# Performance work log

Hardware: AMD Instinct MI355X
Metric: run time of the kernel (lower is better)

Reference implementation:

```python
import jax, jax.numpy as jnp
import numpy as np

N_NODES = 100000


def _lightgcn_layer(x, src, dst, norm):
    # message: norm * x[src]; aggregate: mean over incoming edges at dst
    msg = norm[:, None] * x[src]                                   # [E+N, D]
    s = jax.ops.segment_sum(msg, dst, num_segments=N_NODES)        # [N, D]
    cnt = jax.ops.segment_sum(jnp.ones_like(norm), dst, num_segments=N_NODES)
    return s / cnt[:, None]                                        # deg>=1 due to self-loops


def _graph_embeddings(emb, edge_index):
    n = emb.shape[0]
    loop = jnp.arange(n, dtype=edge_index.dtype)
    src = jnp.concatenate([edge_index[0], loop])                   # self-loops appended
    dst = jnp.concatenate([edge_index[1], loop])
    deg = jax.ops.segment_sum(jnp.ones(src.shape[0], emb.dtype), src, num_segments=N_NODES)
    dis = deg ** -0.5
    norm = dis[src] * dis[dst]
    x = emb
    acc = emb
    for _ in range(2):  # num_layers
        x = _lightgcn_layer(x, src, dst, norm)
        acc = acc + x
    return acc / 3.0  # mean over (num_layers + 1) embeddings


def setup_inputs() -> dict:
    key = jax.random.key(0)
    k1, k2, k3, k4 = jax.random.split(key, 4)
    emb = jax.random.normal(k1, (N_NODES, 128), dtype=jnp.float32) * 0.02
    edge_index = jax.random.randint(k2, (2, 600000), 0, N_NODES, dtype=jnp.int64)
    items = jax.random.randint(k3, (4096, 1), 0, N_NODES, dtype=jnp.int64)
    samples = jax.random.randint(k4, (4096, 100), 0, N_NODES, dtype=jnp.int64)
    return {"emb": emb, "edge_index": edge_index, "items": items, "samples": samples}


def reference(emb, edge_index, items, samples):
    embeddings = _graph_embeddings(emb, edge_index)                # [N, D]
    item_emb = embeddings[items]                                   # [B, 1, D]
    sample_emb = embeddings[samples]                               # [B, S, D]
    scores = jnp.einsum('bod,bsd->bos', item_emb, sample_emb)      # [B, 1, S]
    return scores.squeeze(1)                                       # [B, S]
```

## Files before the change

### kernel.cpp

```cpp
#include <hip/hip_runtime.h>

#define NN 100000
#define D 128
#define W 32
#define NX 8

__device__ __forceinline__ unsigned short f2bf(float f) {
    unsigned u = __float_as_uint(f);
    u += 0x7FFF + ((u >> 16) & 1);
    return (unsigned short)(u >> 16);
}
__device__ __forceinline__ float bf2f(unsigned short h) {
    return __uint_as_float(((unsigned)h) << 16);
}
__device__ __forceinline__ unsigned pack2(float a, float b) {
    return (unsigned)f2bf(a) | ((unsigned)f2bf(b) << 16);
}

__global__ __launch_bounds__(256) void fillcount_kernel(const int* __restrict__ src,
                                                        const int* __restrict__ dst,
                                                        int* __restrict__ degR,
                                                        int* __restrict__ fillc,
                                                        int* __restrict__ ell, int E) {
    int xcc = __builtin_amdgcn_s_getreg(20 | (3 << 11)) & (NX - 1);
    int e = blockIdx.x * 256 + threadIdx.x;
    if (e < E) {
        int s = src[e], d = dst[e];
        __hip_atomic_fetch_add(&degR[(size_t)xcc * NN + s], 1,
                               __ATOMIC_RELAXED, __HIP_MEMORY_SCOPE_WORKGROUP);
        int pos = atomicAdd(&fillc[d], 1);
        if (pos < W) ell[(size_t)d * W + pos] = s;
    }
}

__global__ __launch_bounds__(256) void invert_kernel(const int* __restrict__ degR,
                                                     float* __restrict__ dis,
                                                     float* __restrict__ disinv, int n) {
    int i = blockIdx.x * 256 + threadIdx.x;
    if (i < n) {
        int dsum = 0;
        #pragma unroll
        for (int r = 0; r < NX; ++r) dsum += degR[(size_t)r * NN + i];
        float dp1 = (float)(dsum + 1);
        dis[i] = rsqrtf(dp1);
        disinv[i] = sqrtf(dp1);
    }
}

__global__ __launch_bounds__(256) void convert_kernel(const float* __restrict__ in,
                                                      const float* __restrict__ dis,
                                                      unsigned short* __restrict__ outh,
                                                      int total8) {
    int t = blockIdx.x * 256 + threadIdx.x;
    if (t >= total8) return;
    float sc = dis[t >> 4];
    const float4 a = ((const float4*)in)[t * 2];
    const float4 b = ((const float4*)in)[t * 2 + 1];
    uint4 o;
    o.x = pack2(sc * a.x, sc * a.y);
    o.y = pack2(sc * a.z, sc * a.w);
    o.z = pack2(sc * b.x, sc * b.y);
    o.w = pack2(sc * b.z, sc * b.w);
    ((uint4*)outh)[t] = o;
}

template <bool FUSE>
__global__ __launch_bounds__(256) void gather_kernel(const int* __restrict__ ell,
                                                     const int* __restrict__ fillc,
                                                     const unsigned short* __restrict__ yh,
                                                     const float* __restrict__ emb,
                                                     const float* __restrict__ dis,
                                                     const float* __restrict__ disinv,
                                                     unsigned short* __restrict__ outh, int n) {
    unsigned t = blockIdx.x * 256u + threadIdx.x;
    unsigned i = t >> 5, q = t & 31u;
    if (i >= (unsigned)n) return;
    int len = fillc[i];
    int lenc = len > W ? W : len;
    const int* base = ell + (size_t)i * W;
    const ushort4 ph = *(const ushort4*)(yh + (size_t)i * D + q * 4);
    float sx = bf2f(ph.x), sy = bf2f(ph.y), sz = bf2f(ph.z), sw = bf2f(ph.w);
    float4 acc = {sx, sy, sz, sw};
    int j = 0;
    for (; j + 4 <= lenc; j += 4) {
        const int4 ss = *(const int4*)(base + j);
        const ushort4 v0 = *(const ushort4*)(yh + (size_t)ss.x * D + q * 4);
        const ushort4 v1 = *(const ushort4*)(yh + (size_t)ss.y * D + q * 4);
        const ushort4 v2 = *(const ushort4*)(yh + (size_t)ss.z * D + q * 4);
        const ushort4 v3 = *(const ushort4*)(yh + (size_t)ss.w * D + q * 4);
        acc.x += (bf2f(v0.x) + bf2f(v1.x)) + (bf2f(v2.x) + bf2f(v3.x));
        acc.y += (bf2f(v0.y) + bf2f(v1.y)) + (bf2f(v2.y) + bf2f(v3.y));
        acc.z += (bf2f(v0.z) + bf2f(v1.z)) + (bf2f(v2.z) + bf2f(v3.z));
        acc.w += (bf2f(v0.w) + bf2f(v1.w)) + (bf2f(v2.w) + bf2f(v3.w));
    }
    for (; j < lenc; ++j) {
        int s0 = base[j];
        const ushort4 v0 = *(const ushort4*)(yh + (size_t)s0 * D + q * 4);
        acc.x += bf2f(v0.x);
        acc.y += bf2f(v0.y);
        acc.z += bf2f(v0.z);
        acc.w += bf2f(v0.w);
    }
    float ds = dis[i];
    float ci = 1.0f / (float)(len + 1);
    ushort4 o;
    if (!FUSE) {
        float f1 = ci * ds * ds;
        o.x = f2bf(f1 * acc.x);
        o.y = f2bf(f1 * acc.y);
        o.z = f2bf(f1 * acc.z);
        o.w = f2bf(f1 * acc.w);
    } else {
        float g = ci * ds;
        float dvi = disinv[i];
        const float4 e = *(const float4*)(emb + (size_t)i * D + q * 4);
        const float k = 1.0f / 3.0f;
        o.x = f2bf((e.x + sx * dvi + g * acc.x) * k);
        o.y = f2bf((e.y + sy * dvi + g * acc.y) * k);
        o.z = f2bf((e.z + sz * dvi + g * acc.z) * k);
        o.w = f2bf((e.w + sw * dvi + g * acc.w) * k);
    }
    *(ushort4*)(outh + (size_t)i * D + q * 4) = o;
}

__global__ __launch_bounds__(256) void scores_kernel(const unsigned short* __restrict__ finh,
                                                     const int* __restrict__ items,
                                                     const int* __restrict__ samples,
                                                     float* __restrict__ out, int S) {
    __shared__ float it[D];
    int b = blockIdx.x;
    if (threadIdx.x < D) it[threadIdx.x] = bf2f(finh[(size_t)items[b] * D + threadIdx.x]);
    __syncthreads();
    int hw = threadIdx.x >> 5, lane = threadIdx.x & 31;
    const float4 w = *(const float4*)(it + lane * 4);
    int s = hw;
    for (; s + 8 < S; s += 16) {
        int node0 = samples[b * S + s];
        int node1 = samples[b * S + s + 8];
        const ushort4 v0 = *(const ushort4*)(finh + (size_t)node0 * D + lane * 4);
        const ushort4 v1 = *(const ushort4*)(finh + (size_t)node1 * D + lane * 4);
        float a0 = bf2f(v0.x) * w.x + bf2f(v0.y) * w.y + bf2f(v0.z) * w.z + bf2f(v0.w) * w.w;
        float a1 = bf2f(v1.x) * w.x + bf2f(v1.y) * w.y + bf2f(v1.z) * w.z + bf2f(v1.w) * w.w;
        #pragma unroll
        for (int o = 16; o; o >>= 1) {
            a0 += __shfl_xor(a0, o);
            a1 += __shfl_xor(a1, o);
        }
        if (lane == 0) {
            out[b * S + s] = a0;
            out[b * S + s + 8] = a1;
        }
    }
    if (s < S) {
        int node = samples[b * S + s];
        const ushort4 v = *(const ushort4*)(finh + (size_t)node * D + lane * 4);
        float acc = bf2f(v.x) * w.x + bf2f(v.y) * w.y + bf2f(v.z) * w.z + bf2f(v.w) * w.w;
        #pragma unroll
        for (int o = 16; o; o >>= 1) acc += __shfl_xor(acc, o);
        if (lane == 0) out[b * S + s] = acc;
    }
}

extern "C" void kernel_launch(void* const* d_in, const int* in_sizes, int n_in,
                              void* d_out, int out_size, void* d_ws, size_t ws_size,
                              hipStream_t stream) {
    const float* emb = (const float*)d_in[0];
    const int* ei = (const int*)d_in[1];
    const int* items = (const int*)d_in[2];
    const int* samples = (const int*)d_in[3];
    float* out = (float*)d_out;

    const int E = in_sizes[1] / 2;
    const int B = in_sizes[2];
    const int S = in_sizes[3] / B;
    const int* src = ei;
    const int* dst = ei + E;

    int* degR = (int*)d_ws;
    int* fillc = degR + (size_t)NX * NN;
    float* dis = (float*)(fillc + NN);
    float* disinv = dis + NN;
    int* ell = (int*)(disinv + NN);
    size_t off = (size_t)(ell + (size_t)NN * W - (int*)d_ws);
    off = (off + 3) & ~(size_t)3;
    unsigned short* embh = (unsigned short*)((int*)d_ws + off);
    unsigned short* x1h = embh + (size_t)NN * D;
    unsigned short* finh = x1h + (size_t)NN * D;

    hipMemsetAsync(degR, 0, (NX + 1) * NN * sizeof(int), stream);

    fillcount_kernel<<<(E + 255) / 256, 256, 0, stream>>>(src, dst, degR, fillc, ell, E);
    invert_kernel<<<(NN + 255) / 256, 256, 0, stream>>>(degR, dis, disinv, NN);

    convert_kernel<<<((NN * D / 8) + 255) / 256, 256, 0, stream>>>(emb, dis, embh, NN * D / 8);

    const int gblocks = (NN * 32 + 255) / 256;
    gather_kernel<false><<<gblocks, 256, 0, stream>>>(ell, fillc, embh, emb, dis, disinv, x1h, NN);
    gather_kernel<true><<<gblocks, 256, 0, stream>>>(ell, fillc, x1h, emb, dis, disinv, finh, NN);

    scores_kernel<<<B, 256, 0, stream>>>(finh, items, samples, out, S);
}
```

Before: 174.1 us.

## Merge edge counting with bf16 conversion and compute degree weights inside gather

The edge fill/degree-count pass and the fp32-to-bf16 embedding conversion now run as one heterogeneous launch, split by block index. Because the conversion no longer needs the degree normalization, the separate invert kernel and the per-XCC degree replicas are removed. The first gather applies rsqrt(deg+1) for each neighbor on the fly, which adds a scattered deg load and an rsqrt per edge. Degree atomics are now plain global atomics on a single array, which may increase contention compared with the XCC-replicated counters.

```diff
diff --git a/kernel.cpp b/kernel.cpp
--- a/kernel.cpp
+++ b/kernel.cpp
@@ -3,7 +3,6 @@
 #define NN 100000
 #define D 128
 #define W 32
-#define NX 8
 
 __device__ __forceinline__ unsigned short f2bf(float f) {
     unsigned u = __float_as_uint(f);
@@ -17,77 +16,109 @@
     return (unsigned)f2bf(a) | ((unsigned)f2bf(b) << 16);
 }
 
-__global__ __launch_bounds__(256) void fillcount_kernel(const int* __restrict__ src,
-                                                        const int* __restrict__ dst,
-                                                        int* __restrict__ degR,
-                                                        int* __restrict__ fillc,
-                                                        int* __restrict__ ell, int E) {
-    int xcc = __builtin_amdgcn_s_getreg(20 | (3 << 11)) & (NX - 1);
-    int e = blockIdx.x * 256 + threadIdx.x;
-    if (e < E) {
-        int s = src[e], d = dst[e];
-        __hip_atomic_fetch_add(&degR[(size_t)xcc * NN + s], 1,
-                               __ATOMIC_RELAXED, __HIP_MEMORY_SCOPE_WORKGROUP);
-        int pos = atomicAdd(&fillc[d], 1);
-        if (pos < W) ell[(size_t)d * W + pos] = s;
-    }
-}
-
-__global__ __launch_bounds__(256) void invert_kernel(const int* __restrict__ degR,
-                                                     float* __restrict__ dis,
-                                                     float* __restrict__ disinv, int n) {
-    int i = blockIdx.x * 256 + threadIdx.x;
-    if (i < n) {
-        int dsum = 0;
-        #pragma unroll
-        for (int r = 0; r < NX; ++r) dsum += degR[(size_t)r * NN + i];
-        float dp1 = (float)(dsum + 1);
-        dis[i] = rsqrtf(dp1);
-        disinv[i] = sqrtf(dp1);
-    }
-}
-
-__global__ __launch_bounds__(256) void convert_kernel(const float* __restrict__ in,
-                                                      const float* __restrict__ dis,
-                                                      unsigned short* __restrict__ outh,
-                                                      int total8) {
-    int t = blockIdx.x * 256 + threadIdx.x;
-    if (t >= total8) return;
-    float sc = dis[t >> 4];
-    const float4 a = ((const float4*)in)[t * 2];
-    const float4 b = ((const float4*)in)[t * 2 + 1];
-    uint4 o;
-    o.x = pack2(sc * a.x, sc * a.y);
-    o.y = pack2(sc * a.z, sc * a.w);
-    o.z = pack2(sc * b.x, sc * b.y);
-    o.w = pack2(sc * b.z, sc * b.w);
-    ((uint4*)outh)[t] = o;
-}
-
-template <bool FUSE>
-__global__ __launch_bounds__(256) void gather_kernel(const int* __restrict__ ell,
-                                                     const int* __restrict__ fillc,
-                                                     const unsigned short* __restrict__ yh,
+__global__ __launch_bounds__(256) void hetero_kernel(const int* __restrict__ src,
+                                                     const int* __restrict__ dst,
                                                      const float* __restrict__ emb,
-                                                     const float* __restrict__ dis,
-                                                     const float* __restrict__ disinv,
-                                                     unsigned short* __restrict__ outh, int n) {
+                                                     int* __restrict__ deg,
+                                                     int* __restrict__ fillc,
+                                                     int* __restrict__ ell,
+                                                     unsigned short* __restrict__ y0h,
+                                                     int E, int EB, int total8) {
+    int b = blockIdx.x;
+    if (b < EB) {
+        int e = b * 256 + threadIdx.x;
+        if (e < E) {
+            int s = src[e], d = dst[e];
+            atomicAdd(&deg[s], 1);
+            int pos = atomicAdd(&fillc[d], 1);
+            if (pos < W) ell[(size_t)d * W + pos] = s;
+        }
+    } else {
+        int t = (b - EB) * 256 + threadIdx.x;
+        if (t < total8) {
+            const float4 a = ((const float4*)emb)[t * 2];
+            const float4 c = ((const float4*)emb)[t * 2 + 1];
+            uint4 o;
+            o.x = pack2(a.x, a.y);
+            o.y = pack2(a.z, a.w);
+            o.z = pack2(c.x, c.y);
+            o.w = pack2(c.z, c.w);
+            ((uint4*)y0h)[t] = o;
+        }
+    }
+}
+
+__global__ __launch_bounds__(256) void gather1_kernel(const int* __restrict__ ell,
+                                                      const int* __restrict__ fillc,
+                                                      const int* __restrict__ deg,
+                                                      const unsigned short* __restrict__ y0h,
+                                                      unsigned short* __restrict__ y1h, int n) {
     unsigned t = blockIdx.x * 256u + threadIdx.x;
     unsigned i = t >> 5, q = t & 31u;
     if (i >= (unsigned)n) return;
     int len = fillc[i];
     int lenc = len > W ? W : len;
     const int* base = ell + (size_t)i * W;
-    const ushort4 ph = *(const ushort4*)(yh + (size_t)i * D + q * 4);
+    float wd = rsqrtf((float)deg[i] + 1.0f);
+    const ushort4 ph = *(const ushort4*)(y0h + (size_t)i * D + q * 4);
+    float4 acc = {wd * bf2f(ph.x), wd * bf2f(ph.y), wd * bf2f(ph.z), wd * bf2f(ph.w)};
+    int j = 0;
+    for (; j + 4 <= lenc; j += 4) {
+        const int4 ss = *(const int4*)(base + j);
+        float w0 = rsqrtf((float)deg[ss.x] + 1.0f);
+        float w1 = rsqrtf((float)deg[ss.y] + 1.0f);
+        float w2 = rsqrtf((float)deg[ss.z] + 1.0f);
+        float w3 = rsqrtf((float)deg[ss.w] + 1.0f);
+        const ushort4 v0 = *(const ushort4*)(y0h + (size_t)ss.x * D + q * 4);
+        const ushort4 v1 = *(const ushort4*)(y0h + (size_t)ss.y * D + q * 4);
+        const ushort4 v2 = *(const ushort4*)(y0h + (size_t)ss.z * D + q * 4);
+        const ushort4 v3 = *(const ushort4*)(y0h + (size_t)ss.w * D + q * 4);
+        acc.x += w0 * bf2f(v0.x) + w1 * bf2f(v1.x) + w2 * bf2f(v2.x) + w3 * bf2f(v3.x);
+        acc.y += w0 * bf2f(v0.y) + w1 * bf2f(v1.y) + w2 * bf2f(v2.y) + w3 * bf2f(v3.y);
+        acc.z += w0 * bf2f(v0.z) + w1 * bf2f(v1.z) + w2 * bf2f(v2.z) + w3 * bf2f(v3.z);
+        acc.w += w0 * bf2f(v0.w) + w1 * bf2f(v1.w) + w2 * bf2f(v2.w) + w3 * bf2f(v3.w);
+    }
+    for (; j < lenc; ++j) {
+        int s0 = base[j];
+        float w0 = rsqrtf((float)deg[s0] + 1.0f);
+        const ushort4 v0 = *(const ushort4*)(y0h + (size_t)s0 * D + q * 4);
+        acc.x += w0 * bf2f(v0.x);
+        acc.y += w0 * bf2f(v0.y);
+        acc.z += w0 * bf2f(v0.z);
+        acc.w += w0 * bf2f(v0.w);
+    }
+    float ci = 1.0f / (float)(len + 1);
+    float f1 = ci * wd * wd;
+    ushort4 o;
+    o.x = f2bf(f1 * acc.x);
+    o.y = f2bf(f1 * acc.y);
+    o.z = f2bf(f1 * acc.z);
+    o.w = f2bf(f1 * acc.w);
+    *(ushort4*)(y1h + (size_t)i * D + q * 4) = o;
+}
+
+__global__ __launch_bounds__(256) void gather2_kernel(const int* __restrict__ ell,
+                                                      const int* __restrict__ fillc,
+                                                      const int* __restrict__ deg,
+                                                      const unsigned short* __restrict__ y1h,
+                                                      const float* __restrict__ emb,
+                                                      unsigned short* __restrict__ finh, int n) {
+    unsigned t = blockIdx.x * 256u + threadIdx.x;
+    unsigned i = t >> 5, q = t & 31u;
+    if (i >= (unsigned)n) return;
+    int len = fillc[i];
+    int lenc = len > W ? W : len;
+    const int* base = ell + (size_t)i * W;
+    const ushort4 ph = *(const ushort4*)(y1h + (size_t)i * D + q * 4);
     float sx = bf2f(ph.x), sy = bf2f(ph.y), sz = bf2f(ph.z), sw = bf2f(ph.w);
     float4 acc = {sx, sy, sz, sw};
     int j = 0;
     for (; j + 4 <= lenc; j += 4) {
         const int4 ss = *(const int4*)(base + j);
-        const ushort4 v0 = *(const ushort4*)(yh + (size_t)ss.x * D + q * 4);
-        const ushort4 v1 = *(const ushort4*)(yh + (size_t)ss.y * D + q * 4);
-        const ushort4 v2 = *(const ushort4*)(yh + (size_t)ss.z * D + q * 4);
-        const ushort4 v3 = *(const ushort4*)(yh + (size_t)ss.w * D + q * 4);
+        const ushort4 v0 = *(const ushort4*)(y1h + (size_t)ss.x * D + q * 4);
+        const ushort4 v1 = *(const ushort4*)(y1h + (size_t)ss.y * D + q * 4);
+        const ushort4 v2 = *(const ushort4*)(y1h + (size_t)ss.z * D + q * 4);
+        const ushort4 v3 = *(const ushort4*)(y1h + (size_t)ss.w * D + q * 4);
         acc.x += (bf2f(v0.x) + bf2f(v1.x)) + (bf2f(v2.x) + bf2f(v3.x));
         acc.y += (bf2f(v0.y) + bf2f(v1.y)) + (bf2f(v2.y) + bf2f(v3.y));
         acc.z += (bf2f(v0.z) + bf2f(v1.z)) + (bf2f(v2.z) + bf2f(v3.z));
@@ -95,32 +126,25 @@
     }
     for (; j < lenc; ++j) {
         int s0 = base[j];
-        const ushort4 v0 = *(const ushort4*)(yh + (size_t)s0 * D + q * 4);
+        const ushort4 v0 = *(const ushort4*)(y1h + (size_t)s0 * D + q * 4);
         acc.x += bf2f(v0.x);
         acc.y += bf2f(v0.y);
         acc.z += bf2f(v0.z);
         acc.w += bf2f(v0.w);
     }
-    float ds = dis[i];
+    float dp1 = (float)deg[i] + 1.0f;
+    float wd = rsqrtf(dp1);
+    float wdi = sqrtf(dp1);
     float ci = 1.0f / (float)(len + 1);
+    float g = ci * wd;
+    const float4 e = *(const float4*)(emb + (size_t)i * D + q * 4);
+    const float k = 1.0f / 3.0f;
     ushort4 o;
-    if (!FUSE) {
-        float f1 = ci * ds * ds;
-        o.x = f2bf(f1 * acc.x);
-        o.y = f2bf(f1 * acc.y);
-        o.z = f2bf(f1 * acc.z);
-        o.w = f2bf(f1 * acc.w);
-    } else {
-        float g = ci * ds;
-        float dvi = disinv[i];
-        const float4 e = *(const float4*)(emb + (size_t)i * D + q * 4);
-        const float k = 1.0f / 3.0f;
-        o.x = f2bf((e.x + sx * dvi + g * acc.x) * k);
-        o.y = f2bf((e.y + sy * dvi + g * acc.y) * k);
-        o.z = f2bf((e.z + sz * dvi + g * acc.z) * k);
-        o.w = f2bf((e.w + sw * dvi + g * acc.w) * k);
-    }
-    *(ushort4*)(outh + (size_t)i * D + q * 4) = o;
+    o.x = f2bf((e.x + sx * wdi + g * acc.x) * k);
+    o.y = f2bf((e.y + sy * wdi + g * acc.y) * k);
+    o.z = f2bf((e.z + sz * wdi + g * acc.z) * k);
+    o.w = f2bf((e.w + sw * wdi + g * acc.w) * k);
+    *(ushort4*)(finh + (size_t)i * D + q * 4) = o;
 }
 
 __global__ __launch_bounds__(256) void scores_kernel(const unsigned short* __restrict__ finh,
@@ -176,27 +200,23 @@
     const int* src = ei;
     const int* dst = ei + E;
 
-    int* degR = (int*)d_ws;
-    int* fillc = degR + (size_t)NX * NN;
-    float* dis = (float*)(fillc + NN);
-    float* disinv = dis + NN;
-    int* ell = (int*)(disinv + NN);
-    size_t off = (size_t)(ell + (size_t)NN * W - (int*)d_ws);
-    off = (off + 3) & ~(size_t)3;
-    unsigned short* embh = (unsigned short*)((int*)d_ws + off);
-    unsigned short* x1h = embh + (size_t)NN * D;
-    unsigned short* finh = x1h + (size_t)NN * D;
-
-    hipMemsetAsync(degR, 0, (NX + 1) * NN * sizeof(int), stream);
-
-    fillcount_kernel<<<(E + 255) / 256, 256, 0, stream>>>(src, dst, degR, fillc, ell, E);
-    invert_kernel<<<(NN + 255) / 256, 256, 0, stream>>>(degR, dis, disinv, NN);
-
-    convert_kernel<<<((NN * D / 8) + 255) / 256, 256, 0, stream>>>(emb, dis, embh, NN * D / 8);
+    int* deg = (int*)d_ws;
+    int* fillc = deg + NN;
+    int* ell = fillc + NN;
+    unsigned short* y0h = (unsigned short*)(ell + (size_t)NN * W);
+    unsigned short* y1h = y0h + (size_t)NN * D;
+    unsigned short* finh = y1h + (size_t)NN * D;
+
+    hipMemsetAsync(deg, 0, 2 * NN * sizeof(int), stream);
+
+    const int EB = (E + 255) / 256;
+    const int total8 = NN * D / 8;
+    const int CB = (total8 + 255) / 256;
+    hetero_kernel<<<EB + CB, 256, 0, stream>>>(src, dst, emb, deg, fillc, ell, y0h, E, EB, total8);
 
     const int gblocks = (NN * 32 + 255) / 256;
-    gather_kernel<false><<<gblocks, 256, 0, stream>>>(ell, fillc, embh, emb, dis, disinv, x1h, NN);
-    gather_kernel<true><<<gblocks, 256, 0, stream>>>(ell, fillc, x1h, emb, dis, disinv, finh, NN);
+    gather1_kernel<<<gblocks, 256, 0, stream>>>(ell, fillc, deg, y0h, y1h, NN);
+    gather2_kernel<<<gblocks, 256, 0, stream>>>(ell, fillc, deg, y1h, emb, finh, NN);
 
     scores_kernel<<<B, 256, 0, stream>>>(finh, items, samples, out, S);
 }
```

Result: no change. 172.6 us (-0.9%).
